# Kernel optimization log

Hardware: AMD Instinct MI355X
Metric: run time of the kernel (lower is better)

Reference implementation:

```python
import jax, jax.numpy as jnp
import numpy as np

B, R, N, D_IN, D_OUT = 8, 4, 1024, 256, 256


def setup_inputs() -> dict:
    key = jax.random.key(0)
    k1, k2, k3, k4 = jax.random.split(key, 4)
    text = jax.random.normal(k1, (B, N, D_IN), dtype=jnp.float32)
    adj = jax.random.uniform(k2, (B, R, N, N), dtype=jnp.float32)
    weight = jax.random.normal(k3, (R, D_IN, D_OUT), dtype=jnp.float32) * 0.02
    bias = jax.random.normal(k4, (D_OUT,), dtype=jnp.float32) * 0.02
    return {"text": text, "adj": adj, "weight": weight, "bias": bias}


def reference(text, adj, weight, bias):
    # Row-normalize adjacency per relation (diag_embed+matmul in torch == row scale).
    rowsum = adj.sum(axis=-1)                                   # [B,R,N]
    r_inv = jnp.where(rowsum == 0, 0.0, 1.0 / rowsum)           # inf -> 0
    norm_adj = adj * r_inv[..., None]                           # [B,R,N,N]
    # Per-relation message passing, batched over relations.
    hidden = jnp.einsum('brij,bjd->brid', norm_adj, text)       # [B,R,N,D_in]
    # Concat over relations along feature dim: [B,N,R*D_in]
    tmp = jnp.transpose(hidden, (0, 2, 1, 3)).reshape(text.shape[0], text.shape[1], -1)
    w = weight.reshape(-1, weight.shape[-1])                    # [R*D_in, D_out]
    return tmp @ w + bias
```

## Files before the change

kernel.cpp:

```cpp
#include <hip/hip_runtime.h>
#include <hip/hip_bf16.h>
#include <stdint.h>

typedef __bf16 bf16_8 __attribute__((ext_vector_type(8)));
typedef float f32x4 __attribute__((ext_vector_type(4)));
typedef unsigned int u32;
typedef unsigned short u16;


__device__ __forceinline__ u16 f2b(float f) {
    return __builtin_bit_cast(u16, __float2bfloat16(f));
}

__device__ __forceinline__ u32 swz_off(u32 row, u32 g) {
    return (row * 4u + (g ^ ((row >> 1) & 3u))) * 16u;
}

__device__ __forceinline__ void gload_lds16(const void* g, void* l) {
    __builtin_amdgcn_global_load_lds((const __attribute__((address_space(1))) void*)g,
                                     (__attribute__((address_space(3))) void*)l, 16, 0, 0);
}

__device__ __forceinline__ void memfence_sched() { asm volatile("" ::: "memory"); }

__device__ __forceinline__ uint4 pack8(float4 a, float4 b) {
    uint4 pk;
    pk.x = (u32)f2b(a.x) | ((u32)f2b(a.y) << 16);
    pk.y = (u32)f2b(a.z) | ((u32)f2b(a.w) << 16);
    pk.z = (u32)f2b(b.x) | ((u32)f2b(b.y) << 16);
    pk.w = (u32)f2b(b.z) | ((u32)f2b(b.w) << 16);
    return pk;
}

template <int KSTEPS>
__device__ __forceinline__ void gemm_core(const u16* pA, u32 strideA,
                                          const u16* pB, u32 strideB,
                                          char* smem, f32x4 acc[4][4]) {
    const u32 t    = threadIdx.x;
    const u32 lane = t & 63u;
    const u32 w    = t >> 6;
    const u32 wm   = (w >> 1) * 64u;
    const u32 wn   = (w & 1u) * 64u;
    const u32 waveByte = (t & 192u) * 16u;
    const u32 row0 = t >> 2;
    const u32 gg0  = (t & 3u) ^ ((row0 >> 1) & 3u);
    const u32 row1 = row0 + 64u;
    const u32 gg1  = ((t + 256u) & 3u) ^ ((row1 >> 1) & 3u);
    const u32 fr = lane & 15u;
    const u32 fg = lane >> 4;

    gload_lds16(pA + (size_t)row0 * strideA + gg0 * 8u, smem + waveByte);
    gload_lds16(pA + (size_t)row1 * strideA + gg1 * 8u, smem + waveByte + 4096u);
    gload_lds16(pB + (size_t)row0 * strideB + gg0 * 8u, smem + 16384u + waveByte);
    gload_lds16(pB + (size_t)row1 * strideB + gg1 * 8u, smem + 16384u + waveByte + 4096u);
    asm volatile("s_waitcnt vmcnt(0)" ::: "memory");
    __builtin_amdgcn_s_barrier();

    u32 c = 0;
#pragma unroll 2
    for (int ks = 0; ks < KSTEPS; ++ks) {
        char* curA = smem + c * 8192u;
        char* curB = smem + 16384u + c * 8192u;
        if (ks + 1 < KSTEPS) {
            char* nxtA = smem + (c ^ 1u) * 8192u;
            char* nxtB = smem + 16384u + (c ^ 1u) * 8192u;
            const u32 k0 = (u32)(ks + 1) * 32u;
            gload_lds16(pA + (size_t)row0 * strideA + k0 + gg0 * 8u, nxtA + waveByte);
            gload_lds16(pA + (size_t)row1 * strideA + k0 + gg1 * 8u, nxtA + waveByte + 4096u);
            gload_lds16(pB + (size_t)row0 * strideB + k0 + gg0 * 8u, nxtB + waveByte);
            gload_lds16(pB + (size_t)row1 * strideB + k0 + gg1 * 8u, nxtB + waveByte + 4096u);
        }

        bf16_8 af[4], bfv[4];
#pragma unroll
        for (int mt = 0; mt < 4; ++mt) {
            uint4 v = *(const uint4*)(curA + swz_off(wm + (u32)mt * 16u + fr, fg));
            af[mt] = __builtin_bit_cast(bf16_8, v);
        }
#pragma unroll
        for (int nt = 0; nt < 4; ++nt) {
            uint4 v = *(const uint4*)(curB + swz_off(wn + (u32)nt * 16u + fr, fg));
            bfv[nt] = __builtin_bit_cast(bf16_8, v);
        }
#pragma unroll
        for (int mt = 0; mt < 4; ++mt)
#pragma unroll
            for (int nt = 0; nt < 4; ++nt)
                acc[mt][nt] = __builtin_amdgcn_mfma_f32_16x16x32_bf16(af[mt], bfv[nt],
                                                                      acc[mt][nt], 0, 0, 0);

        if (ks + 1 < KSTEPS) {
            asm volatile("s_waitcnt vmcnt(0)" ::: "memory");
            __builtin_amdgcn_s_barrier();
        }
        c ^= 1u;
    }
}

__global__ __launch_bounds__(256) void text_cvt_kernel(const float* t, u16* tb) {
    const u32 i8 = blockIdx.x * 256u + threadIdx.x;
    const float4 a = ((const float4*)t)[i8 * 2u];
    const float4 b = ((const float4*)t)[i8 * 2u + 1u];
    ((uint4*)tb)[i8] = pack8(a, b);
}

__global__ __launch_bounds__(256) void wt_cvt_kernel(const float* W, u16* Wt) {
    const u32 idx = blockIdx.x * 256u + threadIdx.x;
    const u32 r = idx >> 16, rem = idx & 65535u, dout = rem >> 8, din = rem & 255u;
    Wt[idx] = f2b(W[(r << 16) + (din << 8) + dout]);
}

__global__ __launch_bounds__(256) void y_gemm_kernel(const u16* Wt, const u16* textb,
                                                     u16* Yt) {
    __shared__ char smem[32768];
    const u32 bx = blockIdx.x;
    const u32 n0 = (bx & 7u) * 128u;
    const u32 m0 = ((bx >> 3) & 1u) * 128u;
    const u32 r  = (bx >> 4) & 3u;
    const u32 b  = bx >> 6;
    const u16* pA = Wt + (size_t)r * 65536u + (size_t)m0 * 256u;
    const u16* pB = textb + (size_t)b * 262144u + (size_t)n0 * 256u;
    f32x4 acc[4][4];
#pragma unroll
    for (int i = 0; i < 4; ++i)
#pragma unroll
        for (int j = 0; j < 4; ++j) acc[i][j] = (f32x4){0.f, 0.f, 0.f, 0.f};
    gemm_core<8>(pA, 256u, pB, 256u, smem, acc);

    const u32 lane = threadIdx.x & 63u, w = threadIdx.x >> 6;
    const u32 wm = (w >> 1) * 64u, wn = (w & 1u) * 64u;
    const u32 rit = (lane >> 4) * 4u, cit = lane & 15u;
    u16* yb = Yt + (size_t)(b * 4u + r) * 262144u;
#pragma unroll
    for (int mt = 0; mt < 4; ++mt)
#pragma unroll
        for (int nt = 0; nt < 4; ++nt) {
            const u32 m = m0 + wm + (u32)mt * 16u + rit;
            const u32 n = n0 + wn + (u32)nt * 16u + cit;
#pragma unroll
            for (int rg = 0; rg < 4; ++rg)
                yb[(size_t)(m + (u32)rg) * 1024u + n] = f2b(acc[mt][nt][rg]);
        }
}

__global__ __launch_bounds__(512, 2) void adj_gemm_partial(const float* adj,
                                                           const u16* Yt,
                                                           float* partial) {
    __shared__ char smem[66048];
    char* bufA = smem;
    char* bufB = smem + 16384;
    float* sInv = (float*)(smem + 65536);

    const u32 raw = blockIdx.x;
    const u32 bx = (raw & 7u) * 32u + (raw >> 3);
    const u32 i0 = (bx & 7u) * 128u;
    const u32 r  = (bx >> 3) & 3u;
    const u32 b  = bx >> 5;

    const float* pA = adj + (((size_t)(b * 4u + r)) << 20) + (size_t)i0 * 1024u;
    const u16*   pB = Yt + (((size_t)(b * 4u + r)) << 18);

    const u32 t = threadIdx.x, lane = t & 63u, w = t >> 6;
    const u32 wm = (w >> 2) * 64u;
    const u32 wn = (w & 3u) * 64u;
    const u32 fr = lane & 15u, fg = lane >> 4;

    const u32 sRow = t >> 2;
    const u32 cSwz = (t & 3u) ^ ((sRow >> 1) & 3u);
    const float* aSrc = pA + (size_t)sRow * 1024u + cSwz * 8u;

    const u32 brow0 = t >> 2;
    const u32 brow1 = (t + 512u) >> 2;
    const u32 bg0 = (t & 3u) ^ ((brow0 >> 1) & 3u);
    const u32 bg1 = (t & 3u) ^ ((brow1 >> 1) & 3u);
    const u16* b0p = pB + (size_t)brow0 * 1024u + bg0 * 8u;
    const u16* b1p = pB + (size_t)brow1 * 1024u + bg1 * 8u;
    const u32 waveB = (t & 448u) * 16u;

    f32x4 acc[4][4];
#pragma unroll
    for (int i = 0; i < 4; ++i)
#pragma unroll
        for (int j = 0; j < 4; ++j) acc[i][j] = (f32x4){0.f, 0.f, 0.f, 0.f};

    float s0 = 0.f;
    float4 rA[2][2];

    auto loadA = [&](float4* dst, u32 kt) {
        dst[0] = *(const float4*)(aSrc + kt * 32u);
        dst[1] = *(const float4*)(aSrc + kt * 32u + 4u);
    };
    auto stageB = [&](u32 kt, char* dst) {
        gload_lds16(b0p + kt * 32u, dst + waveB);
        gload_lds16(b1p + kt * 32u, dst + 8192u + waveB);
    };
    auto packA = [&](const float4* a2, char* dst) {
        s0 += (a2[0].x + a2[0].y + a2[0].z + a2[0].w)
            + (a2[1].x + a2[1].y + a2[1].z + a2[1].w);
        *(uint4*)(dst + t * 16u) = pack8(a2[0], a2[1]);
    };
    auto do_mfma = [&](char* curA, char* curB) {
        bf16_8 af[4], bfv[4];
#pragma unroll
        for (int mt = 0; mt < 4; ++mt) {
            uint4 v = *(const uint4*)(curA + swz_off(wm + (u32)mt * 16u + fr, fg));
            af[mt] = __builtin_bit_cast(bf16_8, v);
        }
#pragma unroll
        for (int nt = 0; nt < 4; ++nt) {
            uint4 v = *(const uint4*)(curB + swz_off(wn + (u32)nt * 16u + fr, fg));
            bfv[nt] = __builtin_bit_cast(bf16_8, v);
        }
#pragma unroll
        for (int mt = 0; mt < 4; ++mt)
#pragma unroll
            for (int nt = 0; nt < 4; ++nt)
                acc[mt][nt] = __builtin_amdgcn_mfma_f32_16x16x32_bf16(af[mt], bfv[nt],
                                                                      acc[mt][nt], 0, 0, 0);
    };

    loadA(rA[0], 0u);
    stageB(0u, bufB);
    memfence_sched();
    loadA(rA[1], 1u);
    stageB(1u, bufB + 16384u);
    memfence_sched();
    packA(rA[0], bufA);
    asm volatile("s_waitcnt vmcnt(4) lgkmcnt(0)" ::: "memory");
    __builtin_amdgcn_s_barrier();

#pragma unroll 6
    for (int ks = 0; ks < 30; ++ks) {
        const u32 cA = (u32)ks & 1u, nA = cA ^ 1u;
        packA(rA[nA], bufA + nA * 8192u);
        loadA(rA[cA], (u32)(ks + 2));
        stageB((u32)(ks + 2), bufB + (u32)((ks + 2) % 3) * 16384u);
        do_mfma(bufA + cA * 8192u, bufB + (u32)(ks % 3) * 16384u);
        asm volatile("s_waitcnt vmcnt(4) lgkmcnt(0)" ::: "memory");
        __builtin_amdgcn_s_barrier();
    }
    packA(rA[1], bufA + 8192u);
    do_mfma(bufA, bufB);
    asm volatile("s_waitcnt vmcnt(0) lgkmcnt(0)" ::: "memory");
    __builtin_amdgcn_s_barrier();
    do_mfma(bufA + 8192u, bufB + 16384u);

    s0 += __shfl_down(s0, 2, 64);
    s0 += __shfl_down(s0, 1, 64);
    if ((t & 3u) == 0u) sInv[sRow] = (s0 == 0.f) ? 0.f : 1.f / s0;
    __syncthreads();

    float* pp = partial + (((size_t)(b * 4u + r)) << 18) + (size_t)i0 * 256u;
#pragma unroll
    for (int mt = 0; mt < 4; ++mt)
#pragma unroll
        for (int rg = 0; rg < 4; ++rg) {
            const u32 mRow = wm + (u32)mt * 16u + fg * 4u + (u32)rg;
            const float inv = sInv[mRow];
#pragma unroll
            for (int nt = 0; nt < 4; ++nt)
                pp[(size_t)mRow * 256u + wn + (u32)nt * 16u + fr] = acc[mt][nt][rg] * inv;
        }
}

__global__ __launch_bounds__(256) void reduce_kernel(const float* partial,
                                                     const float* bias, float* out) {
    const u32 i4 = blockIdx.x * 256u + threadIdx.x;
    const u32 base = i4 * 4u;
    const u32 b = base >> 18;
    const u32 rem = base & 262143u;
    float4 s = ((const float4*)bias)[i4 & 63u];
#pragma unroll
    for (u32 r = 0; r < 4; ++r) {
        const float4 v = *(const float4*)(partial + (((size_t)(b * 4u + r)) << 18) + rem);
        s.x += v.x; s.y += v.y; s.z += v.z; s.w += v.w;
    }
    ((float4*)out)[i4] = s;
}

extern "C" void kernel_launch(void* const* d_in, const int* in_sizes, int n_in,
                              void* d_out, int out_size, void* d_ws, size_t ws_size,
                              hipStream_t stream) {
    const float* text = (const float*)d_in[0];
    const float* adj  = (const float*)d_in[1];
    const float* wgt  = (const float*)d_in[2];
    const float* bias = (const float*)d_in[3];
    float* out = (float*)d_out;

    char* ws = (char*)d_ws;
    u16* Yt        = (u16*)ws;
    u16* textb     = (u16*)(ws + 16777216u);
    u16* Wt        = (u16*)(ws + 20971520u);
    float* partial = (float*)(ws + 21495808u);

    text_cvt_kernel<<<1024, 256, 0, stream>>>(text, textb);
    wt_cvt_kernel<<<1024, 256, 0, stream>>>(wgt, Wt);
    y_gemm_kernel<<<512, 256, 0, stream>>>(Wt, textb, Yt);
    adj_gemm_partial<<<256, 512, 0, stream>>>(adj, Yt, partial);
    reduce_kernel<<<2048, 256, 0, stream>>>(partial, bias, out);
}
```

Baseline: 66.06 us.

## Replace partial buffer and reduce pass with atomic accumulation; triple-buffer Y GEMM

The adjacency GEMM now atomically adds its normalized per-relation results straight into the output, which a new kernel pre-fills with the bias. This removes the 32 MB partial write plus the separate reduce kernel that read it back. The Y GEMM is inlined and switched from double to triple buffering with two stages of prefetch, so loads overlap MFMA work better. The price is four-way atomic contention per output element and a float summation order that is no longer deterministic.

New measurement: 80.02 us. 21.1% more time.

```diff
diff --git a/kernel.cpp b/kernel.cpp
--- a/kernel.cpp
+++ b/kernel.cpp
@@ -32,10 +32,38 @@
     return pk;
 }
 
-template <int KSTEPS>
-__device__ __forceinline__ void gemm_core(const u16* pA, u32 strideA,
-                                          const u16* pB, u32 strideB,
-                                          char* smem, f32x4 acc[4][4]) {
+__global__ __launch_bounds__(256) void text_cvt_kernel(const float* t, u16* tb) {
+    const u32 i8 = blockIdx.x * 256u + threadIdx.x;
+    const float4 a = ((const float4*)t)[i8 * 2u];
+    const float4 b = ((const float4*)t)[i8 * 2u + 1u];
+    ((uint4*)tb)[i8] = pack8(a, b);
+}
+
+__global__ __launch_bounds__(256) void wt_cvt_kernel(const float* W, u16* Wt) {
+    const u32 idx = blockIdx.x * 256u + threadIdx.x;
+    const u32 r = idx >> 16, rem = idx & 65535u, dout = rem >> 8, din = rem & 255u;
+    Wt[idx] = f2b(W[(r << 16) + (din << 8) + dout]);
+}
+
+__global__ __launch_bounds__(256) void bias_fill_kernel(const float* bias, float* out) {
+    const u32 i4 = blockIdx.x * 256u + threadIdx.x;
+    ((float4*)out)[i4] = ((const float4*)bias)[i4 & 63u];
+}
+
+__global__ __launch_bounds__(256) void y_gemm_kernel(const u16* Wt, const u16* textb,
+                                                     u16* Yt) {
+    __shared__ char smem[49152];
+    char* bufA = smem;
+    char* bufB = smem + 24576;
+
+    const u32 bx = blockIdx.x;
+    const u32 n0 = (bx & 7u) * 128u;
+    const u32 m0 = ((bx >> 3) & 1u) * 128u;
+    const u32 r  = (bx >> 4) & 3u;
+    const u32 b  = bx >> 6;
+    const u16* pA = Wt + (size_t)r * 65536u + (size_t)m0 * 256u;
+    const u16* pB = textb + (size_t)b * 262144u + (size_t)n0 * 256u;
+
     const u32 t    = threadIdx.x;
     const u32 lane = t & 63u;
     const u32 w    = t >> 6;
@@ -49,28 +77,27 @@
     const u32 fr = lane & 15u;
     const u32 fg = lane >> 4;
 
-    gload_lds16(pA + (size_t)row0 * strideA + gg0 * 8u, smem + waveByte);
-    gload_lds16(pA + (size_t)row1 * strideA + gg1 * 8u, smem + waveByte + 4096u);
-    gload_lds16(pB + (size_t)row0 * strideB + gg0 * 8u, smem + 16384u + waveByte);
-    gload_lds16(pB + (size_t)row1 * strideB + gg1 * 8u, smem + 16384u + waveByte + 4096u);
-    asm volatile("s_waitcnt vmcnt(0)" ::: "memory");
-    __builtin_amdgcn_s_barrier();
-
-    u32 c = 0;
-#pragma unroll 2
-    for (int ks = 0; ks < KSTEPS; ++ks) {
-        char* curA = smem + c * 8192u;
-        char* curB = smem + 16384u + c * 8192u;
-        if (ks + 1 < KSTEPS) {
-            char* nxtA = smem + (c ^ 1u) * 8192u;
-            char* nxtB = smem + 16384u + (c ^ 1u) * 8192u;
-            const u32 k0 = (u32)(ks + 1) * 32u;
-            gload_lds16(pA + (size_t)row0 * strideA + k0 + gg0 * 8u, nxtA + waveByte);
-            gload_lds16(pA + (size_t)row1 * strideA + k0 + gg1 * 8u, nxtA + waveByte + 4096u);
-            gload_lds16(pB + (size_t)row0 * strideB + k0 + gg0 * 8u, nxtB + waveByte);
-            gload_lds16(pB + (size_t)row1 * strideB + k0 + gg1 * 8u, nxtB + waveByte + 4096u);
-        }
-
+    const u16* a0p = pA + (size_t)row0 * 256u + gg0 * 8u;
+    const u16* a1p = pA + (size_t)row1 * 256u + gg1 * 8u;
+    const u16* b0p = pB + (size_t)row0 * 256u + gg0 * 8u;
+    const u16* b1p = pB + (size_t)row1 * 256u + gg1 * 8u;
+
+    f32x4 acc[4][4];
+#pragma unroll
+    for (int i = 0; i < 4; ++i)
+#pragma unroll
+        for (int j = 0; j < 4; ++j) acc[i][j] = (f32x4){0.f, 0.f, 0.f, 0.f};
+
+    auto stage = [&](u32 ks, u32 slot) {
+        const u32 k0 = ks * 32u;
+        gload_lds16(a0p + k0, bufA + slot * 8192u + waveByte);
+        gload_lds16(a1p + k0, bufA + slot * 8192u + waveByte + 4096u);
+        gload_lds16(b0p + k0, bufB + slot * 8192u + waveByte);
+        gload_lds16(b1p + k0, bufB + slot * 8192u + waveByte + 4096u);
+    };
+    auto do_mfma = [&](u32 slot) {
+        char* curA = bufA + slot * 8192u;
+        char* curB = bufB + slot * 8192u;
         bf16_8 af[4], bfv[4];
 #pragma unroll
         for (int mt = 0; mt < 4; ++mt) {
@@ -88,48 +115,29 @@
             for (int nt = 0; nt < 4; ++nt)
                 acc[mt][nt] = __builtin_amdgcn_mfma_f32_16x16x32_bf16(af[mt], bfv[nt],
                                                                       acc[mt][nt], 0, 0, 0);
-
-        if (ks + 1 < KSTEPS) {
-            asm volatile("s_waitcnt vmcnt(0)" ::: "memory");
-            __builtin_amdgcn_s_barrier();
-        }
-        c ^= 1u;
+    };
+
+    stage(0u, 0u);
+    memfence_sched();
+    stage(1u, 1u);
+    memfence_sched();
+    asm volatile("s_waitcnt vmcnt(4)" ::: "memory");
+    __builtin_amdgcn_s_barrier();
+
+#pragma unroll 6
+    for (int ks = 0; ks < 6; ++ks) {
+        stage((u32)(ks + 2), (u32)((ks + 2) % 3));
+        memfence_sched();
+        do_mfma((u32)(ks % 3));
+        asm volatile("s_waitcnt vmcnt(4) lgkmcnt(0)" ::: "memory");
+        __builtin_amdgcn_s_barrier();
     }
-}
-
-__global__ __launch_bounds__(256) void text_cvt_kernel(const float* t, u16* tb) {
-    const u32 i8 = blockIdx.x * 256u + threadIdx.x;
-    const float4 a = ((const float4*)t)[i8 * 2u];
-    const float4 b = ((const float4*)t)[i8 * 2u + 1u];
-    ((uint4*)tb)[i8] = pack8(a, b);
-}
-
-__global__ __launch_bounds__(256) void wt_cvt_kernel(const float* W, u16* Wt) {
-    const u32 idx = blockIdx.x * 256u + threadIdx.x;
-    const u32 r = idx >> 16, rem = idx & 65535u, dout = rem >> 8, din = rem & 255u;
-    Wt[idx] = f2b(W[(r << 16) + (din << 8) + dout]);
-}
-
-__global__ __launch_bounds__(256) void y_gemm_kernel(const u16* Wt, const u16* textb,
-                                                     u16* Yt) {
-    __shared__ char smem[32768];
-    const u32 bx = blockIdx.x;
-    const u32 n0 = (bx & 7u) * 128u;
-    const u32 m0 = ((bx >> 3) & 1u) * 128u;
-    const u32 r  = (bx >> 4) & 3u;
-    const u32 b  = bx >> 6;
-    const u16* pA = Wt + (size_t)r * 65536u + (size_t)m0 * 256u;
-    const u16* pB = textb + (size_t)b * 262144u + (size_t)n0 * 256u;
-    f32x4 acc[4][4];
-#pragma unroll
-    for (int i = 0; i < 4; ++i)
-#pragma unroll
-        for (int j = 0; j < 4; ++j) acc[i][j] = (f32x4){0.f, 0.f, 0.f, 0.f};
-    gemm_core<8>(pA, 256u, pB, 256u, smem, acc);
-
-    const u32 lane = threadIdx.x & 63u, w = threadIdx.x >> 6;
-    const u32 wm = (w >> 1) * 64u, wn = (w & 1u) * 64u;
-    const u32 rit = (lane >> 4) * 4u, cit = lane & 15u;
+    do_mfma(0u);
+    asm volatile("s_waitcnt vmcnt(0) lgkmcnt(0)" ::: "memory");
+    __builtin_amdgcn_s_barrier();
+    do_mfma(1u);
+
+    const u32 rit = fg * 4u, cit = fr;
     u16* yb = Yt + (size_t)(b * 4u + r) * 262144u;
 #pragma unroll
     for (int mt = 0; mt < 4; ++mt)
@@ -143,9 +151,9 @@
         }
 }
 
-__global__ __launch_bounds__(512, 2) void adj_gemm_partial(const float* adj,
-                                                           const u16* Yt,
-                                                           float* partial) {
+__global__ __launch_bounds__(512, 2) void adj_gemm_atomic(const float* adj,
+                                                          const u16* Yt,
+                                                          float* out) {
     __shared__ char smem[66048];
     char* bufA = smem;
     char* bufB = smem + 16384;
@@ -250,7 +258,7 @@
     if ((t & 3u) == 0u) sInv[sRow] = (s0 == 0.f) ? 0.f : 1.f / s0;
     __syncthreads();
 
-    float* pp = partial + (((size_t)(b * 4u + r)) << 18) + (size_t)i0 * 256u;
+    float* ob = out + ((size_t)b << 18) + (size_t)i0 * 256u;
 #pragma unroll
     for (int mt = 0; mt < 4; ++mt)
 #pragma unroll
@@ -259,23 +267,9 @@
             const float inv = sInv[mRow];
 #pragma unroll
             for (int nt = 0; nt < 4; ++nt)
-                pp[(size_t)mRow * 256u + wn + (u32)nt * 16u + fr] = acc[mt][nt][rg] * inv;
-        }
-}
-
-__global__ __launch_bounds__(256) void reduce_kernel(const float* partial,
-                                                     const float* bias, float* out) {
-    const u32 i4 = blockIdx.x * 256u + threadIdx.x;
-    const u32 base = i4 * 4u;
-    const u32 b = base >> 18;
-    const u32 rem = base & 262143u;
-    float4 s = ((const float4*)bias)[i4 & 63u];
-#pragma unroll
-    for (u32 r = 0; r < 4; ++r) {
-        const float4 v = *(const float4*)(partial + (((size_t)(b * 4u + r)) << 18) + rem);
-        s.x += v.x; s.y += v.y; s.z += v.z; s.w += v.w;
-    }
-    ((float4*)out)[i4] = s;
+                unsafeAtomicAdd(&ob[(size_t)mRow * 256u + wn + (u32)nt * 16u + fr],
+                                acc[mt][nt][rg] * inv);
+        }
 }
 
 extern "C" void kernel_launch(void* const* d_in, const int* in_sizes, int n_in,
@@ -288,14 +282,13 @@
     float* out = (float*)d_out;
 
     char* ws = (char*)d_ws;
-    u16* Yt        = (u16*)ws;
-    u16* textb     = (u16*)(ws + 16777216u);
-    u16* Wt        = (u16*)(ws + 20971520u);
-    float* partial = (float*)(ws + 21495808u);
-
+    u16* Yt    = (u16*)ws;
+    u16* textb = (u16*)(ws + 16777216u);
+    u16* Wt    = (u16*)(ws + 20971520u);
+
+    bias_fill_kernel<<<2048, 256, 0, stream>>>(bias, out);
     text_cvt_kernel<<<1024, 256, 0, stream>>>(text, textb);
     wt_cvt_kernel<<<1024, 256, 0, stream>>>(wgt, Wt);
     y_gemm_kernel<<<512, 256, 0, stream>>>(Wt, textb, Yt);
-    adj_gemm_partial<<<256, 512, 0, stream>>>(adj, Yt, partial);
-    reduce_kernel<<<2048, 256, 0, stream>>>(partial, bias, out);
-}
+    adj_gemm_atomic<<<256, 512, 0, stream>>>(adj, Yt, out);
+}
```
